# Performance work log

Hardware: AMD Instinct MI355X
Metric: run time of the kernel (lower is better)

The kernel has to match this reference:

```python
import jax, jax.numpy as jnp
import numpy as np


def _warp_nn(img, flow):
    """Nearest-neighbor warp of one sample.
    img:  [C, D, H, W] channels to deform
    flow: [3, D, H, W] voxel displacements for dims (D, H, W)
    out(p) = img(round(p + flow(p))), indices clamped to the volume.
    """
    D, H, W = img.shape[1:]
    gd = jnp.arange(D, dtype=flow.dtype)[:, None, None]
    gh = jnp.arange(H, dtype=flow.dtype)[None, :, None]
    gw = jnp.arange(W, dtype=flow.dtype)[None, None, :]
    id_ = jnp.clip(jnp.round(gd + flow[0]), 0, D - 1).astype(jnp.int32)
    ih = jnp.clip(jnp.round(gh + flow[1]), 0, H - 1).astype(jnp.int32)
    iw = jnp.clip(jnp.round(gw + flow[2]), 0, W - 1).astype(jnp.int32)
    return img[:, id_, ih, iw]  # gather, [C, D, H, W]


def reference(x, num_steps):
    # scaling: v = x / 2**num_steps
    B, C = x.shape[0], x.shape[1]
    spatial = x.shape[2:]
    v = x / (2.0 ** num_steps)
    # squaring: v <- v + warp(v, v), applied per 3-channel flow group
    warp = jax.vmap(jax.vmap(_warp_nn))  # over batch, then over groups
    for _ in range(num_steps):
        groups = v.reshape(B, C // 3, 3, *spatial)
        vdef = warp(groups, groups).reshape(v.shape)
        v = v + vdef
    return v


def setup_inputs() -> dict:
    key = jax.random.key(0)
    # displacement field in voxel units; scaled so post-scaling steps still move voxels
    x = jax.random.normal(key, (2, 3, 128, 160, 160), dtype=jnp.float32) * 8.0
    return {"x": x, "num_steps": 6}
```

## Files before the change

kernel.cpp:

```cpp
#include <hip/hip_runtime.h>

#define BB 2
#define DD 128
#define HH 160
#define WW 160
constexpr int S   = DD * HH * WW;
constexpr int PL  = HH * WW;
constexpr int VPB = 512;
constexpr int BPP = PL / VPB;
constexpr int NBLK = BB * DD * BPP;
constexpr int PER_XCD = NBLK / 8;

__device__ __forceinline__ int warp_index(int d, int h, int w,
                                          float f0, float f1, float f2) {
    int id = (int)fminf(fmaxf(rintf((float)d + f0), 0.0f), (float)(DD - 1));
    int ih = (int)fminf(fmaxf(rintf((float)h + f1), 0.0f), (float)(HH - 1));
    int iw = (int)fminf(fmaxf(rintf((float)w + f2), 0.0f), (float)(WW - 1));
    return (id * HH + ih) * WW + iw;
}

template <bool IN_SOA, bool OUT_SOA>
__global__ __launch_bounds__(256) void step_k(const float* __restrict__ vin,
                                              float* __restrict__ vout,
                                              float scale) {
    int bid = blockIdx.x;
    int nb  = (bid >> 3) + (bid & 7) * PER_XCD;
    int b   = nb / (DD * BPP);
    int r   = nb - b * (DD * BPP);
    int d   = r / BPP;
    int ip0 = (r - d * BPP) * VPB + threadIdx.x;
    int ip1 = ip0 + 256;

    int w0 = ip0 % WW, h0 = ip0 / WW;
    int w1 = ip1 % WW, h1 = ip1 / WW;
    int p0 = d * PL + ip0;
    int p1 = d * PL + ip1;

    float a0, a1, a2, c0, c1, c2;
    if constexpr (IN_SOA) {
        int s0 = b * 3 * S + p0, s1 = b * 3 * S + p1;
        a0 = vin[s0] * scale; a1 = vin[s0 + S] * scale; a2 = vin[s0 + 2 * S] * scale;
        c0 = vin[s1] * scale; c1 = vin[s1 + S] * scale; c2 = vin[s1 + 2 * S] * scale;
    } else {
        int i0 = (b * S + p0) * 3, i1 = (b * S + p1) * 3;
        a0 = vin[i0] * scale; a1 = vin[i0 + 1] * scale; a2 = vin[i0 + 2] * scale;
        c0 = vin[i1] * scale; c1 = vin[i1 + 1] * scale; c2 = vin[i1 + 2] * scale;
    }

    int q0 = warp_index(d, h0, w0, a0, a1, a2);
    int q1 = warp_index(d, h1, w1, c0, c1, c2);

    float g0, g1, g2, e0, e1, e2;
    if constexpr (IN_SOA) {
        int s0 = b * 3 * S + q0, s1 = b * 3 * S + q1;
        g0 = vin[s0] * scale; g1 = vin[s0 + S] * scale; g2 = vin[s0 + 2 * S] * scale;
        e0 = vin[s1] * scale; e1 = vin[s1 + S] * scale; e2 = vin[s1 + 2 * S] * scale;
    } else {
        int i0 = (b * S + q0) * 3, i1 = (b * S + q1) * 3;
        g0 = vin[i0] * scale; g1 = vin[i0 + 1] * scale; g2 = vin[i0 + 2] * scale;
        e0 = vin[i1] * scale; e1 = vin[i1 + 1] * scale; e2 = vin[i1 + 2] * scale;
    }

    if constexpr (OUT_SOA) {
        int s0 = b * 3 * S + p0, s1 = b * 3 * S + p1;
        vout[s0] = a0 + g0; vout[s0 + S] = a1 + g1; vout[s0 + 2 * S] = a2 + g2;
        vout[s1] = c0 + e0; vout[s1 + S] = c1 + e1; vout[s1 + 2 * S] = c2 + e2;
    } else {
        int i0 = (b * S + p0) * 3, i1 = (b * S + p1) * 3;
        vout[i0] = a0 + g0; vout[i0 + 1] = a1 + g1; vout[i0 + 2] = a2 + g2;
        vout[i1] = c0 + e0; vout[i1 + 1] = c1 + e1; vout[i1 + 2] = c2 + e2;
    }
}

extern "C" void kernel_launch(void* const* d_in, const int* in_sizes, int n_in,
                              void* d_out, int out_size, void* d_ws, size_t ws_size,
                              hipStream_t stream) {
    const float* x = (const float*)d_in[0];
    float* out = (float*)d_out;
    float* ws  = (float*)d_ws;

    step_k<true,  false><<<NBLK, 256, 0, stream>>>(x,   ws,  1.0f / 64.0f);
    step_k<false, false><<<NBLK, 256, 0, stream>>>(ws,  out, 1.0f);
    step_k<false, false><<<NBLK, 256, 0, stream>>>(out, ws,  1.0f);
    step_k<false, false><<<NBLK, 256, 0, stream>>>(ws,  out, 1.0f);
    step_k<false, false><<<NBLK, 256, 0, stream>>>(out, ws,  1.0f);
    step_k<false, true ><<<NBLK, 256, 0, stream>>>(ws,  out, 1.0f);
}
```

Measured before the change: 267.7 us.

## Fuse pairs of squaring steps into one kernel by recomputing neighbor values

Each new kernel computes two squaring steps at once. It recomputes the intermediate value at the warped location with chained gathers from the input field, so the intermediate field is never written. This halves the number of launches and full-field write/read passes, in exchange for four dependent gathers per voxel instead of two. It also needs a workspace large enough for two fields and falls back to the old six-launch path otherwise.

New measurement: 281.5 us. +5.2%, slower.

```diff
diff --git a/kernel.cpp b/kernel.cpp
--- a/kernel.cpp
+++ b/kernel.cpp
@@ -11,12 +11,78 @@
 constexpr int NBLK = BB * DD * BPP;
 constexpr int PER_XCD = NBLK / 8;
 
-__device__ __forceinline__ int warp_index(int d, int h, int w,
+struct I3 { int d, h, w; };
+
+__device__ __forceinline__ I3 warp_coords(int d, int h, int w,
                                           float f0, float f1, float f2) {
-    int id = (int)fminf(fmaxf(rintf((float)d + f0), 0.0f), (float)(DD - 1));
-    int ih = (int)fminf(fmaxf(rintf((float)h + f1), 0.0f), (float)(HH - 1));
-    int iw = (int)fminf(fmaxf(rintf((float)w + f2), 0.0f), (float)(WW - 1));
-    return (id * HH + ih) * WW + iw;
+    I3 r;
+    r.d = (int)fminf(fmaxf(rintf((float)d + f0), 0.0f), (float)(DD - 1));
+    r.h = (int)fminf(fmaxf(rintf((float)h + f1), 0.0f), (float)(HH - 1));
+    r.w = (int)fminf(fmaxf(rintf((float)w + f2), 0.0f), (float)(WW - 1));
+    return r;
+}
+
+template <bool SOA>
+__device__ __forceinline__ void load3(const float* __restrict__ v, int b, int idx,
+                                      float s, float& o0, float& o1, float& o2) {
+    if constexpr (SOA) {
+        int i = b * 3 * S + idx;
+        o0 = v[i] * s; o1 = v[i + S] * s; o2 = v[i + 2 * S] * s;
+    } else {
+        int i = (b * S + idx) * 3;
+        o0 = v[i] * s; o1 = v[i + 1] * s; o2 = v[i + 2] * s;
+    }
+}
+
+template <bool IN_SOA>
+__device__ __forceinline__ void fused2(const float* __restrict__ vin, int b,
+                                       int d, int h, int w, float scale,
+                                       float& o0, float& o1, float& o2) {
+    int p = (d * HH + h) * WW + w;
+    float f0, f1, f2;
+    load3<IN_SOA>(vin, b, p, scale, f0, f1, f2);
+    I3 q = warp_coords(d, h, w, f0, f1, f2);
+    float g0, g1, g2;
+    load3<IN_SOA>(vin, b, (q.d * HH + q.h) * WW + q.w, scale, g0, g1, g2);
+    float v10 = f0 + g0, v11 = f1 + g1, v12 = f2 + g2;
+    I3 r = warp_coords(d, h, w, v10, v11, v12);
+    float fr0, fr1, fr2;
+    load3<IN_SOA>(vin, b, (r.d * HH + r.h) * WW + r.w, scale, fr0, fr1, fr2);
+    I3 qr = warp_coords(r.d, r.h, r.w, fr0, fr1, fr2);
+    float gr0, gr1, gr2;
+    load3<IN_SOA>(vin, b, (qr.d * HH + qr.h) * WW + qr.w, scale, gr0, gr1, gr2);
+    float v1r0 = fr0 + gr0, v1r1 = fr1 + gr1, v1r2 = fr2 + gr2;
+    o0 = v10 + v1r0; o1 = v11 + v1r1; o2 = v12 + v1r2;
+}
+
+template <bool IN_SOA, bool OUT_SOA>
+__global__ __launch_bounds__(256) void step2_k(const float* __restrict__ vin,
+                                               float* __restrict__ vout,
+                                               float scale) {
+    int bid = blockIdx.x;
+    int nb  = (bid >> 3) + (bid & 7) * PER_XCD;
+    int b   = nb / (DD * BPP);
+    int rr  = nb - b * (DD * BPP);
+    int d   = rr / BPP;
+    int ip0 = (rr - d * BPP) * VPB + threadIdx.x;
+    int ip1 = ip0 + 256;
+    int w0 = ip0 % WW, h0 = ip0 / WW;
+    int w1 = ip1 % WW, h1 = ip1 / WW;
+
+    float a0, a1, a2, c0, c1, c2;
+    fused2<IN_SOA>(vin, b, d, h0, w0, scale, a0, a1, a2);
+    fused2<IN_SOA>(vin, b, d, h1, w1, scale, c0, c1, c2);
+
+    int p0 = d * PL + ip0, p1 = d * PL + ip1;
+    if constexpr (OUT_SOA) {
+        int s0 = b * 3 * S + p0, s1 = b * 3 * S + p1;
+        vout[s0] = a0; vout[s0 + S] = a1; vout[s0 + 2 * S] = a2;
+        vout[s1] = c0; vout[s1 + S] = c1; vout[s1 + 2 * S] = c2;
+    } else {
+        int i0 = (b * S + p0) * 3, i1 = (b * S + p1) * 3;
+        vout[i0] = a0; vout[i0 + 1] = a1; vout[i0 + 2] = a2;
+        vout[i1] = c0; vout[i1 + 1] = c1; vout[i1 + 2] = c2;
+    }
 }
 
 template <bool IN_SOA, bool OUT_SOA>
@@ -26,49 +92,25 @@
     int bid = blockIdx.x;
     int nb  = (bid >> 3) + (bid & 7) * PER_XCD;
     int b   = nb / (DD * BPP);
-    int r   = nb - b * (DD * BPP);
-    int d   = r / BPP;
-    int ip0 = (r - d * BPP) * VPB + threadIdx.x;
-    int ip1 = ip0 + 256;
-
-    int w0 = ip0 % WW, h0 = ip0 / WW;
-    int w1 = ip1 % WW, h1 = ip1 / WW;
-    int p0 = d * PL + ip0;
-    int p1 = d * PL + ip1;
-
-    float a0, a1, a2, c0, c1, c2;
-    if constexpr (IN_SOA) {
-        int s0 = b * 3 * S + p0, s1 = b * 3 * S + p1;
-        a0 = vin[s0] * scale; a1 = vin[s0 + S] * scale; a2 = vin[s0 + 2 * S] * scale;
-        c0 = vin[s1] * scale; c1 = vin[s1 + S] * scale; c2 = vin[s1 + 2 * S] * scale;
-    } else {
-        int i0 = (b * S + p0) * 3, i1 = (b * S + p1) * 3;
-        a0 = vin[i0] * scale; a1 = vin[i0 + 1] * scale; a2 = vin[i0 + 2] * scale;
-        c0 = vin[i1] * scale; c1 = vin[i1 + 1] * scale; c2 = vin[i1 + 2] * scale;
-    }
-
-    int q0 = warp_index(d, h0, w0, a0, a1, a2);
-    int q1 = warp_index(d, h1, w1, c0, c1, c2);
-
-    float g0, g1, g2, e0, e1, e2;
-    if constexpr (IN_SOA) {
-        int s0 = b * 3 * S + q0, s1 = b * 3 * S + q1;
-        g0 = vin[s0] * scale; g1 = vin[s0 + S] * scale; g2 = vin[s0 + 2 * S] * scale;
-        e0 = vin[s1] * scale; e1 = vin[s1 + S] * scale; e2 = vin[s1 + 2 * S] * scale;
-    } else {
-        int i0 = (b * S + q0) * 3, i1 = (b * S + q1) * 3;
-        g0 = vin[i0] * scale; g1 = vin[i0 + 1] * scale; g2 = vin[i0 + 2] * scale;
-        e0 = vin[i1] * scale; e1 = vin[i1 + 1] * scale; e2 = vin[i1 + 2] * scale;
-    }
-
-    if constexpr (OUT_SOA) {
-        int s0 = b * 3 * S + p0, s1 = b * 3 * S + p1;
-        vout[s0] = a0 + g0; vout[s0 + S] = a1 + g1; vout[s0 + 2 * S] = a2 + g2;
-        vout[s1] = c0 + e0; vout[s1 + S] = c1 + e1; vout[s1 + 2 * S] = c2 + e2;
-    } else {
-        int i0 = (b * S + p0) * 3, i1 = (b * S + p1) * 3;
-        vout[i0] = a0 + g0; vout[i0 + 1] = a1 + g1; vout[i0 + 2] = a2 + g2;
-        vout[i1] = c0 + e0; vout[i1 + 1] = c1 + e1; vout[i1 + 2] = c2 + e2;
+    int rr  = nb - b * (DD * BPP);
+    int d   = rr / BPP;
+    int ip0 = (rr - d * BPP) * VPB + threadIdx.x;
+    for (int v = 0; v < 2; ++v) {
+        int ip = ip0 + v * 256;
+        int w = ip % WW, h = ip / WW;
+        int p = d * PL + ip;
+        float f0, f1, f2;
+        load3<IN_SOA>(vin, b, p, scale, f0, f1, f2);
+        I3 q = warp_coords(d, h, w, f0, f1, f2);
+        float g0, g1, g2;
+        load3<IN_SOA>(vin, b, (q.d * HH + q.h) * WW + q.w, scale, g0, g1, g2);
+        if constexpr (OUT_SOA) {
+            int s0 = b * 3 * S + p;
+            vout[s0] = f0 + g0; vout[s0 + S] = f1 + g1; vout[s0 + 2 * S] = f2 + g2;
+        } else {
+            int i0 = (b * S + p) * 3;
+            vout[i0] = f0 + g0; vout[i0 + 1] = f1 + g1; vout[i0 + 2] = f2 + g2;
+        }
     }
 }
 
@@ -79,10 +121,21 @@
     float* out = (float*)d_out;
     float* ws  = (float*)d_ws;
 
-    step_k<true,  false><<<NBLK, 256, 0, stream>>>(x,   ws,  1.0f / 64.0f);
-    step_k<false, false><<<NBLK, 256, 0, stream>>>(ws,  out, 1.0f);
-    step_k<false, false><<<NBLK, 256, 0, stream>>>(out, ws,  1.0f);
-    step_k<false, false><<<NBLK, 256, 0, stream>>>(ws,  out, 1.0f);
-    step_k<false, false><<<NBLK, 256, 0, stream>>>(out, ws,  1.0f);
-    step_k<false, true ><<<NBLK, 256, 0, stream>>>(ws,  out, 1.0f);
+    const size_t fieldf = (size_t)BB * S * 3;
+    const size_t need   = 2 * fieldf * sizeof(float);
+
+    if (ws_size >= need) {
+        float* A = ws;
+        float* B = ws + fieldf;
+        step2_k<true,  false><<<NBLK, 256, 0, stream>>>(x, A, 1.0f / 64.0f);
+        step2_k<false, false><<<NBLK, 256, 0, stream>>>(A, B, 1.0f);
+        step2_k<false, true ><<<NBLK, 256, 0, stream>>>(B, out, 1.0f);
+    } else {
+        step_k<true,  false><<<NBLK, 256, 0, stream>>>(x,   ws,  1.0f / 64.0f);
+        step_k<false, false><<<NBLK, 256, 0, stream>>>(ws,  out, 1.0f);
+        step_k<false, false><<<NBLK, 256, 0, stream>>>(out, ws,  1.0f);
+        step_k<false, false><<<NBLK, 256, 0, stream>>>(ws,  out, 1.0f);
+        step_k<false, false><<<NBLK, 256, 0, stream>>>(out, ws,  1.0f);
+        step_k<false, true ><<<NBLK, 256, 0, stream>>>(ws,  out, 1.0f);
+    }
 }
```

## Fuse first three squaring steps into one kernel via recursive recomputation

Applied to the files above, without the earlier changes.

Replaces the first three warp-and-add launches with one kernel that recomputes intermediate fields on the fly by recursively evaluating v1 and v2 at warped positions directly from the input. This removes the writes and reads of two intermediate fields and two launches. In exchange, each voxel performs many more dependent random gathers. The remaining steps use 12-byte packed loads and stores and a separate workspace ping-pong buffer.

Measured after the change: 331.3 us. +23.8%, slower.

```diff
diff --git a/kernel.cpp b/kernel.cpp
--- a/kernel.cpp
+++ b/kernel.cpp
@@ -11,64 +11,101 @@
 constexpr int NBLK = BB * DD * BPP;
 constexpr int PER_XCD = NBLK / 8;
 
-__device__ __forceinline__ int warp_index(int d, int h, int w,
-                                          float f0, float f1, float f2) {
-    int id = (int)fminf(fmaxf(rintf((float)d + f0), 0.0f), (float)(DD - 1));
-    int ih = (int)fminf(fmaxf(rintf((float)h + f1), 0.0f), (float)(HH - 1));
-    int iw = (int)fminf(fmaxf(rintf((float)w + f2), 0.0f), (float)(WW - 1));
-    return (id * HH + ih) * WW + iw;
+struct I3 { int d, h, w; };
+struct F3 { float x, y, z; };
+
+__device__ __forceinline__ I3 warp_coords(int d, int h, int w, F3 f) {
+    I3 r;
+    r.d = (int)fminf(fmaxf(rintf((float)d + f.x), 0.0f), (float)(DD - 1));
+    r.h = (int)fminf(fmaxf(rintf((float)h + f.y), 0.0f), (float)(HH - 1));
+    r.w = (int)fminf(fmaxf(rintf((float)w + f.z), 0.0f), (float)(WW - 1));
+    return r;
 }
 
-template <bool IN_SOA, bool OUT_SOA>
-__global__ __launch_bounds__(256) void step_k(const float* __restrict__ vin,
-                                              float* __restrict__ vout,
-                                              float scale) {
+__device__ __forceinline__ F3 ld3(const float* p) {
+    F3 r; __builtin_memcpy(&r, p, 12); return r;
+}
+__device__ __forceinline__ void st3(float* p, F3 v) {
+    __builtin_memcpy(p, &v, 12);
+}
+
+__device__ __forceinline__ F3 ld_soa(const float* __restrict__ xb, int d, int h, int w) {
+    const float scale = 1.0f / 64.0f;
+    int i = (d * HH + h) * WW + w;
+    F3 r; r.x = xb[i] * scale; r.y = xb[i + S] * scale; r.z = xb[i + 2 * S] * scale;
+    return r;
+}
+
+__device__ __forceinline__ F3 v1_at(const float* __restrict__ xb, int d, int h, int w) {
+    F3 f = ld_soa(xb, d, h, w);
+    I3 q = warp_coords(d, h, w, f);
+    F3 g = ld_soa(xb, q.d, q.h, q.w);
+    return {f.x + g.x, f.y + g.y, f.z + g.z};
+}
+
+__device__ __forceinline__ F3 v2_at(const float* __restrict__ xb, int d, int h, int w) {
+    F3 a = v1_at(xb, d, h, w);
+    I3 r = warp_coords(d, h, w, a);
+    F3 b = v1_at(xb, r.d, r.h, r.w);
+    return {a.x + b.x, a.y + b.y, a.z + b.z};
+}
+
+__device__ __forceinline__ F3 v3_at(const float* __restrict__ xb, int d, int h, int w) {
+    F3 a = v2_at(xb, d, h, w);
+    I3 r = warp_coords(d, h, w, a);
+    F3 b = v2_at(xb, r.d, r.h, r.w);
+    return {a.x + b.x, a.y + b.y, a.z + b.z};
+}
+
+__global__ __launch_bounds__(256) void fused3_k(const float* __restrict__ x,
+                                                float* __restrict__ vout) {
     int bid = blockIdx.x;
     int nb  = (bid >> 3) + (bid & 7) * PER_XCD;
     int b   = nb / (DD * BPP);
-    int r   = nb - b * (DD * BPP);
-    int d   = r / BPP;
-    int ip0 = (r - d * BPP) * VPB + threadIdx.x;
+    int rr  = nb - b * (DD * BPP);
+    int d   = rr / BPP;
+    int ip0 = (rr - d * BPP) * VPB + threadIdx.x;
+    const float* xb = x + b * 3 * S;
+
+    for (int v = 0; v < 2; ++v) {
+        int ip = ip0 + v * 256;
+        int w = ip % WW, h = ip / WW;
+        F3 o = v3_at(xb, d, h, w);
+        st3(vout + (size_t)(b * S + d * PL + ip) * 3, o);
+    }
+}
+
+template <bool OUT_SOA>
+__global__ __launch_bounds__(256) void step_k(const float* __restrict__ vin,
+                                              float* __restrict__ vout) {
+    int bid = blockIdx.x;
+    int nb  = (bid >> 3) + (bid & 7) * PER_XCD;
+    int b   = nb / (DD * BPP);
+    int rr  = nb - b * (DD * BPP);
+    int d   = rr / BPP;
+    int ip0 = (rr - d * BPP) * VPB + threadIdx.x;
     int ip1 = ip0 + 256;
-
     int w0 = ip0 % WW, h0 = ip0 / WW;
     int w1 = ip1 % WW, h1 = ip1 / WW;
-    int p0 = d * PL + ip0;
-    int p1 = d * PL + ip1;
+    int p0 = d * PL + ip0, p1 = d * PL + ip1;
 
-    float a0, a1, a2, c0, c1, c2;
-    if constexpr (IN_SOA) {
-        int s0 = b * 3 * S + p0, s1 = b * 3 * S + p1;
-        a0 = vin[s0] * scale; a1 = vin[s0 + S] * scale; a2 = vin[s0 + 2 * S] * scale;
-        c0 = vin[s1] * scale; c1 = vin[s1 + S] * scale; c2 = vin[s1 + 2 * S] * scale;
-    } else {
-        int i0 = (b * S + p0) * 3, i1 = (b * S + p1) * 3;
-        a0 = vin[i0] * scale; a1 = vin[i0 + 1] * scale; a2 = vin[i0 + 2] * scale;
-        c0 = vin[i1] * scale; c1 = vin[i1 + 1] * scale; c2 = vin[i1 + 2] * scale;
-    }
+    F3 f0 = ld3(vin + (size_t)(b * S + p0) * 3);
+    F3 f1 = ld3(vin + (size_t)(b * S + p1) * 3);
+    I3 q0 = warp_coords(d, h0, w0, f0);
+    I3 q1 = warp_coords(d, h1, w1, f1);
+    F3 g0 = ld3(vin + (size_t)(b * S + (q0.d * HH + q0.h) * WW + q0.w) * 3);
+    F3 g1 = ld3(vin + (size_t)(b * S + (q1.d * HH + q1.h) * WW + q1.w) * 3);
 
-    int q0 = warp_index(d, h0, w0, a0, a1, a2);
-    int q1 = warp_index(d, h1, w1, c0, c1, c2);
-
-    float g0, g1, g2, e0, e1, e2;
-    if constexpr (IN_SOA) {
-        int s0 = b * 3 * S + q0, s1 = b * 3 * S + q1;
-        g0 = vin[s0] * scale; g1 = vin[s0 + S] * scale; g2 = vin[s0 + 2 * S] * scale;
-        e0 = vin[s1] * scale; e1 = vin[s1 + S] * scale; e2 = vin[s1 + 2 * S] * scale;
-    } else {
-        int i0 = (b * S + q0) * 3, i1 = (b * S + q1) * 3;
-        g0 = vin[i0] * scale; g1 = vin[i0 + 1] * scale; g2 = vin[i0 + 2] * scale;
-        e0 = vin[i1] * scale; e1 = vin[i1 + 1] * scale; e2 = vin[i1 + 2] * scale;
-    }
+    F3 o0 = {f0.x + g0.x, f0.y + g0.y, f0.z + g0.z};
+    F3 o1 = {f1.x + g1.x, f1.y + g1.y, f1.z + g1.z};
 
     if constexpr (OUT_SOA) {
         int s0 = b * 3 * S + p0, s1 = b * 3 * S + p1;
-        vout[s0] = a0 + g0; vout[s0 + S] = a1 + g1; vout[s0 + 2 * S] = a2 + g2;
-        vout[s1] = c0 + e0; vout[s1 + S] = c1 + e1; vout[s1 + 2 * S] = c2 + e2;
+        vout[s0] = o0.x; vout[s0 + S] = o0.y; vout[s0 + 2 * S] = o0.z;
+        vout[s1] = o1.x; vout[s1 + S] = o1.y; vout[s1 + 2 * S] = o1.z;
     } else {
-        int i0 = (b * S + p0) * 3, i1 = (b * S + p1) * 3;
-        vout[i0] = a0 + g0; vout[i0 + 1] = a1 + g1; vout[i0 + 2] = a2 + g2;
-        vout[i1] = c0 + e0; vout[i1 + 1] = c1 + e1; vout[i1 + 2] = c2 + e2;
+        st3(vout + (size_t)(b * S + p0) * 3, o0);
+        st3(vout + (size_t)(b * S + p1) * 3, o1);
     }
 }
 
@@ -79,10 +116,12 @@
     float* out = (float*)d_out;
     float* ws  = (float*)d_ws;
 
-    step_k<true,  false><<<NBLK, 256, 0, stream>>>(x,   ws,  1.0f / 64.0f);
-    step_k<false, false><<<NBLK, 256, 0, stream>>>(ws,  out, 1.0f);
-    step_k<false, false><<<NBLK, 256, 0, stream>>>(out, ws,  1.0f);
-    step_k<false, false><<<NBLK, 256, 0, stream>>>(ws,  out, 1.0f);
-    step_k<false, false><<<NBLK, 256, 0, stream>>>(out, ws,  1.0f);
-    step_k<false, true ><<<NBLK, 256, 0, stream>>>(ws,  out, 1.0f);
+    const size_t fieldf = (size_t)BB * S * 3;
+    float* A = ws;
+    float* B = (ws_size >= 2 * fieldf * sizeof(float)) ? (ws + fieldf) : out;
+
+    fused3_k      <<<NBLK, 256, 0, stream>>>(x, A);
+    step_k<false> <<<NBLK, 256, 0, stream>>>(A, B);
+    step_k<false> <<<NBLK, 256, 0, stream>>>(B, A);
+    step_k<true>  <<<NBLK, 256, 0, stream>>>(A, out);
 }
```

## Vectorize warp step to 4 voxels per thread with wave-uniform identity-gather skip

Applied to the files above, without the earlier changes.

Each thread now handles 4 consecutive voxels, loading and storing them with float4 accesses in both SoA and interleaved layouts instead of scalar accesses. When every lane's rounded target equals its own voxel, the wave skips the gather and reuses the loaded values. The scale becomes a compile-time template flag, and a second workspace buffer is used when ws_size allows. The aim is fewer memory instructions and less gather traffic, at the cost of fewer blocks and more registers per thread.

Result: slower. 309.7 us (+15.7%).

```diff
diff --git a/kernel.cpp b/kernel.cpp
--- a/kernel.cpp
+++ b/kernel.cpp
@@ -6,69 +6,108 @@
 #define WW 160
 constexpr int S   = DD * HH * WW;
 constexpr int PL  = HH * WW;
-constexpr int VPB = 512;
+constexpr int VPT = 4;
+constexpr int VPB = 256 * VPT;
 constexpr int BPP = PL / VPB;
 constexpr int NBLK = BB * DD * BPP;
 constexpr int PER_XCD = NBLK / 8;
 
-__device__ __forceinline__ int warp_index(int d, int h, int w,
+struct I3 { int d, h, w; };
+
+__device__ __forceinline__ I3 warp_coords(int d, int h, int w,
                                           float f0, float f1, float f2) {
-    int id = (int)fminf(fmaxf(rintf((float)d + f0), 0.0f), (float)(DD - 1));
-    int ih = (int)fminf(fmaxf(rintf((float)h + f1), 0.0f), (float)(HH - 1));
-    int iw = (int)fminf(fmaxf(rintf((float)w + f2), 0.0f), (float)(WW - 1));
-    return (id * HH + ih) * WW + iw;
+    I3 r;
+    r.d = (int)fminf(fmaxf(rintf((float)d + f0), 0.0f), (float)(DD - 1));
+    r.h = (int)fminf(fmaxf(rintf((float)h + f1), 0.0f), (float)(HH - 1));
+    r.w = (int)fminf(fmaxf(rintf((float)w + f2), 0.0f), (float)(WW - 1));
+    return r;
 }
 
-template <bool IN_SOA, bool OUT_SOA>
+template <bool IN_SOA, bool OUT_SOA, bool SCALE>
 __global__ __launch_bounds__(256) void step_k(const float* __restrict__ vin,
-                                              float* __restrict__ vout,
-                                              float scale) {
+                                              float* __restrict__ vout) {
     int bid = blockIdx.x;
     int nb  = (bid >> 3) + (bid & 7) * PER_XCD;
     int b   = nb / (DD * BPP);
-    int r   = nb - b * (DD * BPP);
-    int d   = r / BPP;
-    int ip0 = (r - d * BPP) * VPB + threadIdx.x;
-    int ip1 = ip0 + 256;
+    int rr  = nb - b * (DD * BPP);
+    int d   = rr / BPP;
+    int blk = rr - d * BPP;
+    int ip  = blk * VPB + threadIdx.x * VPT;
+    int w0  = ip % WW;
+    int h   = ip / WW;
+    int p   = d * PL + ip;
 
-    int w0 = ip0 % WW, h0 = ip0 / WW;
-    int w1 = ip1 % WW, h1 = ip1 / WW;
-    int p0 = d * PL + ip0;
-    int p1 = d * PL + ip1;
+    const float scale = 1.0f / 64.0f;
 
-    float a0, a1, a2, c0, c1, c2;
+    float f[12];
     if constexpr (IN_SOA) {
-        int s0 = b * 3 * S + p0, s1 = b * 3 * S + p1;
-        a0 = vin[s0] * scale; a1 = vin[s0 + S] * scale; a2 = vin[s0 + 2 * S] * scale;
-        c0 = vin[s1] * scale; c1 = vin[s1 + S] * scale; c2 = vin[s1 + 2 * S] * scale;
+        const float* xb = vin + b * 3 * S;
+        float4 u0 = *(const float4*)(xb + p);
+        float4 u1 = *(const float4*)(xb + S + p);
+        float4 u2 = *(const float4*)(xb + 2 * S + p);
+        f[0]=u0.x; f[3]=u0.y; f[6]=u0.z; f[9] =u0.w;
+        f[1]=u1.x; f[4]=u1.y; f[7]=u1.z; f[10]=u1.w;
+        f[2]=u2.x; f[5]=u2.y; f[8]=u2.z; f[11]=u2.w;
     } else {
-        int i0 = (b * S + p0) * 3, i1 = (b * S + p1) * 3;
-        a0 = vin[i0] * scale; a1 = vin[i0 + 1] * scale; a2 = vin[i0 + 2] * scale;
-        c0 = vin[i1] * scale; c1 = vin[i1 + 1] * scale; c2 = vin[i1 + 2] * scale;
+        const float4* src = (const float4*)(vin + (size_t)(b * S + p) * 3);
+        float4 a = src[0], c4 = src[1], e = src[2];
+        f[0]=a.x; f[1]=a.y; f[2]=a.z;  f[3]=a.w;
+        f[4]=c4.x;f[5]=c4.y;f[6]=c4.z; f[7]=c4.w;
+        f[8]=e.x; f[9]=e.y; f[10]=e.z; f[11]=e.w;
+    }
+    if constexpr (SCALE) {
+#pragma unroll
+        for (int i = 0; i < 12; ++i) f[i] *= scale;
     }
 
-    int q0 = warp_index(d, h0, w0, a0, a1, a2);
-    int q1 = warp_index(d, h1, w1, c0, c1, c2);
-
-    float g0, g1, g2, e0, e1, e2;
-    if constexpr (IN_SOA) {
-        int s0 = b * 3 * S + q0, s1 = b * 3 * S + q1;
-        g0 = vin[s0] * scale; g1 = vin[s0 + S] * scale; g2 = vin[s0 + 2 * S] * scale;
-        e0 = vin[s1] * scale; e1 = vin[s1 + S] * scale; e2 = vin[s1 + 2 * S] * scale;
-    } else {
-        int i0 = (b * S + q0) * 3, i1 = (b * S + q1) * 3;
-        g0 = vin[i0] * scale; g1 = vin[i0 + 1] * scale; g2 = vin[i0 + 2] * scale;
-        e0 = vin[i1] * scale; e1 = vin[i1 + 1] * scale; e2 = vin[i1 + 2] * scale;
+    I3 q[4];
+    bool neq = false;
+#pragma unroll
+    for (int c = 0; c < 4; ++c) {
+        q[c] = warp_coords(d, h, w0 + c, f[3*c], f[3*c+1], f[3*c+2]);
+        neq |= (q[c].d != d) | (q[c].h != h) | (q[c].w != (w0 + c));
     }
 
+    float g[12];
+    if (__ballot(neq)) {
+#pragma unroll
+        for (int c = 0; c < 4; ++c) {
+            int qi = (q[c].d * HH + q[c].h) * WW + q[c].w;
+            if constexpr (IN_SOA) {
+                const float* xb = vin + b * 3 * S;
+                g[3*c]   = xb[qi];
+                g[3*c+1] = xb[qi + S];
+                g[3*c+2] = xb[qi + 2 * S];
+            } else {
+                const float* sp = vin + (size_t)(b * S + qi) * 3;
+                float t[3];
+                __builtin_memcpy(t, sp, 12);
+                g[3*c] = t[0]; g[3*c+1] = t[1]; g[3*c+2] = t[2];
+            }
+        }
+        if constexpr (SCALE) {
+#pragma unroll
+            for (int i = 0; i < 12; ++i) g[i] *= scale;
+        }
+    } else {
+#pragma unroll
+        for (int i = 0; i < 12; ++i) g[i] = f[i];
+    }
+
+    float o[12];
+#pragma unroll
+    for (int i = 0; i < 12; ++i) o[i] = f[i] + g[i];
+
     if constexpr (OUT_SOA) {
-        int s0 = b * 3 * S + p0, s1 = b * 3 * S + p1;
-        vout[s0] = a0 + g0; vout[s0 + S] = a1 + g1; vout[s0 + 2 * S] = a2 + g2;
-        vout[s1] = c0 + e0; vout[s1 + S] = c1 + e1; vout[s1 + 2 * S] = c2 + e2;
+        float* ob = vout + b * 3 * S;
+        *(float4*)(ob + p)         = make_float4(o[0], o[3], o[6], o[9]);
+        *(float4*)(ob + S + p)     = make_float4(o[1], o[4], o[7], o[10]);
+        *(float4*)(ob + 2 * S + p) = make_float4(o[2], o[5], o[8], o[11]);
     } else {
-        int i0 = (b * S + p0) * 3, i1 = (b * S + p1) * 3;
-        vout[i0] = a0 + g0; vout[i0 + 1] = a1 + g1; vout[i0 + 2] = a2 + g2;
-        vout[i1] = c0 + e0; vout[i1 + 1] = c1 + e1; vout[i1 + 2] = c2 + e2;
+        float4* dst = (float4*)(vout + (size_t)(b * S + p) * 3);
+        dst[0] = make_float4(o[0], o[1], o[2],  o[3]);
+        dst[1] = make_float4(o[4], o[5], o[6],  o[7]);
+        dst[2] = make_float4(o[8], o[9], o[10], o[11]);
     }
 }
 
@@ -79,10 +118,14 @@
     float* out = (float*)d_out;
     float* ws  = (float*)d_ws;
 
-    step_k<true,  false><<<NBLK, 256, 0, stream>>>(x,   ws,  1.0f / 64.0f);
-    step_k<false, false><<<NBLK, 256, 0, stream>>>(ws,  out, 1.0f);
-    step_k<false, false><<<NBLK, 256, 0, stream>>>(out, ws,  1.0f);
-    step_k<false, false><<<NBLK, 256, 0, stream>>>(ws,  out, 1.0f);
-    step_k<false, false><<<NBLK, 256, 0, stream>>>(out, ws,  1.0f);
-    step_k<false, true ><<<NBLK, 256, 0, stream>>>(ws,  out, 1.0f);
+    const size_t fieldf = (size_t)BB * S * 3;
+    float* A = ws;
+    float* B = (ws_size >= 2 * fieldf * sizeof(float)) ? (ws + fieldf) : out;
+
+    step_k<true,  false, true ><<<NBLK, 256, 0, stream>>>(x, A);
+    step_k<false, false, false><<<NBLK, 256, 0, stream>>>(A, B);
+    step_k<false, false, false><<<NBLK, 256, 0, stream>>>(B, A);
+    step_k<false, false, false><<<NBLK, 256, 0, stream>>>(A, B);
+    step_k<false, false, false><<<NBLK, 256, 0, stream>>>(B, A);
+    step_k<false, true,  false><<<NBLK, 256, 0, stream>>>(A, out);
 }
```
